# Optimization experiments

Hardware: AMD Instinct MI355X
Metric: run time of the kernel (lower is better)

Reference implementation:

```python
import jax, jax.numpy as jnp
import numpy as np

N = 50000
E = 800000
G = 8  # number of graphs
D_IN, D_H, D_OUT = 300, 128, 64


def _linear_params(key, d_out, d_in):
    k1, k2 = jax.random.split(key)
    s = 1.0 / np.sqrt(d_in)
    W = jax.random.uniform(k1, (d_out, d_in), minval=-s, maxval=s, dtype=jnp.float32)
    b = jax.random.uniform(k2, (d_out,), minval=-s, maxval=s, dtype=jnp.float32)
    return W, b


def setup_inputs() -> dict:
    key = jax.random.key(0)
    ks = jax.random.split(key, 10)
    x = jax.random.normal(ks[0], (N, D_IN), dtype=jnp.float32)
    edge_index = jax.random.randint(ks[1], (2, E), 0, N, dtype=jnp.int64)
    batch = jnp.sort(jax.random.randint(ks[2], (N,), 0, G, dtype=jnp.int64))
    W_emb, b_emb = _linear_params(ks[3], D_H, D_IN)
    # SAGEConv layer 0: lin_l (neighbors, with bias), lin_r (root, no bias)
    Wl0, bl0 = _linear_params(ks[4], D_H, D_H)
    Wr0, _ = _linear_params(ks[5], D_H, D_H)
    # SAGEConv layer 1
    Wl1, bl1 = _linear_params(ks[6], D_H, D_H)
    Wr1, _ = _linear_params(ks[7], D_H, D_H)
    W_att, b_att = _linear_params(ks[8], 1, D_H)
    W_out, b_out = _linear_params(ks[9], D_OUT, D_H)
    return {
        "x": x, "edge_index": edge_index, "batch": batch,
        "W_emb": W_emb, "b_emb": b_emb,
        "Wl0": Wl0, "bl0": bl0, "Wr0": Wr0,
        "Wl1": Wl1, "bl1": bl1, "Wr1": Wr1,
        "W_att": W_att, "b_att": b_att,
        "W_out": W_out, "b_out": b_out,
    }


def _sage_conv(h, src, dst, Wl, bl, Wr):
    # mean aggregation of source-node features onto destination nodes
    agg = jax.ops.segment_sum(h[src], dst, num_segments=N)  # [N, D_H]
    deg = jax.ops.segment_sum(jnp.ones((src.shape[0],), dtype=h.dtype), dst, num_segments=N)
    agg = agg / jnp.maximum(deg, 1.0)[:, None]
    return agg @ Wl.T + bl + h @ Wr.T


def reference(x, edge_index, batch, W_emb, b_emb, Wl0, bl0, Wr0, Wl1, bl1, Wr1,
              W_att, b_att, W_out, b_out):
    src, dst = edge_index[0], edge_index[1]
    h = x @ W_emb.T + b_emb                       # [N, D_H]
    h = jax.nn.relu(_sage_conv(h, src, dst, Wl0, bl0, Wr0))
    h = jax.nn.relu(_sage_conv(h, src, dst, Wl1, bl1, Wr1))
    # attention readout: softmax over ALL nodes (dim=0), as in original code
    scores = h @ W_att.T + b_att                  # [N, 1]
    weights = jax.nn.softmax(scores, axis=0)      # [N, 1]
    pooled = jax.ops.segment_sum(h * weights, batch, num_segments=G)  # [G, D_H]
    return pooled @ W_out.T + b_out               # [G, D_OUT]
```

## Files before the change

kernel.cpp:

```cpp
#include <hip/hip_runtime.h>
#include <math.h>

#define D_H 128

typedef __attribute__((ext_vector_type(8))) __bf16 bf16x8;
typedef __attribute__((ext_vector_type(4))) float f32x4;

__device__ __forceinline__ void split_bf16(float v, unsigned short& hi, unsigned short& lo) {
  unsigned int u = __float_as_uint(v);
  hi = (unsigned short)(u >> 16);
  float l = v - __uint_as_float(u & 0xffff0000u);
  lo = (unsigned short)(__float_as_uint(l) >> 16);
}

__device__ __forceinline__ float blo(unsigned int u) { return __uint_as_float(u << 16); }
__device__ __forceinline__ float bhi(unsigned int u) { return __uint_as_float(u & 0xffff0000u); }

__device__ __forceinline__ void pack_pair8(const float* xv, bf16x8& ah, bf16x8& al) {
  union { bf16x8 v; unsigned int u[4]; } H, L;
#pragma unroll
  for (int e = 0; e < 4; ++e) {
    unsigned int u0 = __float_as_uint(xv[2 * e]);
    unsigned int u1 = __float_as_uint(xv[2 * e + 1]);
    float l0 = xv[2 * e] - __uint_as_float(u0 & 0xffff0000u);
    float l1 = xv[2 * e + 1] - __uint_as_float(u1 & 0xffff0000u);
    H.u[e] = (u0 >> 16) | (u1 & 0xffff0000u);
    L.u[e] = (__float_as_uint(l0) >> 16) | (__float_as_uint(l1) & 0xffff0000u);
  }
  ah = H.v;
  al = L.v;
}

__device__ __forceinline__ void load_lds16(const void* g, void* l) {
  __builtin_amdgcn_global_load_lds((const __attribute__((address_space(1))) unsigned int*)g,
                                   (__attribute__((address_space(3))) unsigned int*)l,
                                   16, 0, 0);
}


__global__ __launch_bounds__(256) void k_histw(
    const int* __restrict__ dstv, int* __restrict__ bucketCnt, int E,
    const float* __restrict__ Wemb, const float* __restrict__ Wl0,
    const float* __restrict__ Wr0, const float* __restrict__ Wl1,
    const float* __restrict__ Wr1, unsigned short* __restrict__ WembP,
    unsigned short* __restrict__ P0l, unsigned short* __restrict__ P0r,
    unsigned short* __restrict__ P1l, unsigned short* __restrict__ P1r) {
  __shared__ int h[256];
  int t = threadIdx.x;
  h[t] = 0;
  __syncthreads();
  for (int i = blockIdx.x * 256 + t; i < E; i += gridDim.x * 256)
    atomicAdd(&h[dstv[i] >> 8], 1);

  int tid = blockIdx.x * 256 + t;
  const int EMB = 128 * 320;
  if (tid < EMB) {
    int o = tid / 320, k = tid - o * 320;
    float v = (k < 300) ? Wemb[o * 300 + k] : 0.f;
    unsigned short hh, ll;
    split_bf16(v, hh, ll);
    int sw = ((2 * k) ^ ((o & 7) << 4)) >> 1;
    WembP[o * 640 + sw] = hh;
    WembP[o * 640 + 320 + sw] = ll;
  } else if (tid < EMB + 4 * 16384) {
    int r = tid - EMB;
    int m = r >> 14;
    int i = r & 16383;
    int o = i >> 7, k = i & 127;
    const float* W = (m == 0) ? Wl0 : (m == 1) ? Wr0 : (m == 2) ? Wl1 : Wr1;
    unsigned short* P = (m == 0) ? P0l : (m == 1) ? P0r : (m == 2) ? P1l : P1r;
    unsigned short hh, ll;
    split_bf16(W[o * 128 + k], hh, ll);
    int sw = ((2 * k) ^ ((o & 7) << 4)) >> 1;
    P[o * 256 + sw] = hh;
    P[o * 256 + 128 + sw] = ll;
  }

  __syncthreads();
  if (h[t]) atomicAdd(&bucketCnt[t], h[t]);
}

__global__ __launch_bounds__(256) void k_bucketscan(const int* __restrict__ bucketCnt, int NB,
                                                    int* __restrict__ bucketBase,
                                                    int* __restrict__ cursor,
                                                    int* __restrict__ row_ptr, int N, int E) {
  __shared__ int s[256];
  int t = threadIdx.x;
  int v = (t < NB) ? bucketCnt[t] : 0;
  s[t] = v;
  __syncthreads();
  for (int off = 1; off < 256; off <<= 1) {
    int u = (t >= off) ? s[t - off] : 0;
    __syncthreads();
    s[t] += u;
    __syncthreads();
  }
  int excl = s[t] - v;
  if (t < NB) {
    bucketBase[t] = excl;
    cursor[t] = excl;
  }
  if (t == NB - 1) bucketBase[NB] = excl + v;
  if (t == 0) row_ptr[N] = E;
}

__global__ __launch_bounds__(256) void k_binscatter(const int* __restrict__ srcv,
                                                    const int* __restrict__ dstv,
                                                    int* __restrict__ cursor,
                                                    unsigned int* __restrict__ tmp, int E) {
  __shared__ int h[256];
  __shared__ int base[256];
  int t = threadIdx.x;
  int chunk = (E + gridDim.x - 1) / gridDim.x;
  int c0 = blockIdx.x * chunk;
  int c1 = min(c0 + chunk, E);
  int dst[16], src[16];
  h[t] = 0;
  __syncthreads();
#pragma unroll
  for (int p = 0; p < 16; ++p) {
    int i = c0 + p * 256 + t;
    if (i < c1) {
      dst[p] = dstv[i];
      src[p] = srcv[i];
      atomicAdd(&h[dst[p] >> 8], 1);
    } else {
      dst[p] = -1;
      src[p] = 0;
    }
  }
  __syncthreads();
  int cnt = h[t];
  __syncthreads();
  base[t] = cnt ? atomicAdd(&cursor[t], cnt) : 0;
  h[t] = 0;
  __syncthreads();
#pragma unroll
  for (int p = 0; p < 16; ++p) {
    if (dst[p] >= 0) {
      int b = dst[p] >> 8;
      int pos = base[b] + atomicAdd(&h[b], 1);
      tmp[pos] = (unsigned int)src[p] | ((unsigned int)(dst[p] & 255) << 16);
    }
  }
}

__global__ __launch_bounds__(256) void k_localcsr(const unsigned int* __restrict__ tmp,
                                                  const int* __restrict__ bucketBase,
                                                  int* __restrict__ row_ptr,
                                                  int* __restrict__ col, int N) {
  __shared__ int deg[256], rp[256], cur[256];
  int b = blockIdx.x, t = threadIdx.x;
  int s = bucketBase[b], e = bucketBase[b + 1];
  int epb = e - s;
  deg[t] = 0;
  __syncthreads();
  for (int i = t; i < epb; i += 256) atomicAdd(&deg[tmp[s + i] >> 16], 1);
  __syncthreads();
  int v = deg[t];
  rp[t] = v;
  __syncthreads();
  for (int off = 1; off < 256; off <<= 1) {
    int u = (t >= off) ? rp[t - off] : 0;
    __syncthreads();
    rp[t] += u;
    __syncthreads();
  }
  int excl = rp[t] - v;
  rp[t] = excl;
  cur[t] = 0;
  int gid = b * 256 + t;
  if (gid < N) row_ptr[gid] = s + excl;
  __syncthreads();
  for (int i = t; i < epb; i += 256) {
    unsigned int p = tmp[s + i];
    int dl = p >> 16;
    int pos = s + rp[dl] + atomicAdd(&cur[dl], 1);
    col[pos] = (int)(p & 0xffffu);
  }
}


__global__ __launch_bounds__(512, 4) void k_emb(const float* __restrict__ x,
                                                const unsigned short* __restrict__ Wp,
                                                const float* __restrict__ bias,
                                                unsigned short* __restrict__ P, int N) {
  __shared__ alignas(16) char sW[34048];
  int t = threadIdx.x, lane = t & 63, wave = t >> 6;
  int row0 = blockIdx.x * 128;
  int fr = lane & 15, q4 = lane >> 4;
  int X = (fr & 7) << 4;
  int row = row0 + wave * 16 + fr;
  if (row >= N) row = N - 1;
  const float* xrp = x + (size_t)row * 300;
  f32x4 acc[8] = {};
  float xb[2][8];

  auto loadx = [&](float* d, int c0) {
    if (c0 + 7 < 300) {
      float4 a = *(const float4*)(xrp + c0);
      float4 b = *(const float4*)(xrp + c0 + 4);
      d[0] = a.x; d[1] = a.y; d[2] = a.z; d[3] = a.w;
      d[4] = b.x; d[5] = b.y; d[6] = b.z; d[7] = b.w;
    } else {
#pragma unroll
      for (int e = 0; e < 8; ++e) d[e] = (c0 + e < 300) ? xrp[c0 + e] : 0.f;
    }
  };

  loadx(xb[0], q4 * 8);
#pragma unroll
  for (int kc = 0; kc < 5; ++kc) {
#pragma unroll
    for (int r = 0; r < 4; ++r) {
      int off = r * 8192 + wave * 1024;
      int offl = off + lane * 16;
      int c = offl >> 8;
      int w = offl & 255;
      const char* src = (const char*)Wp + (size_t)c * 1280 +
                        (w < 128 ? kc * 128 + w : 640 + kc * 128 + (w - 128));
      load_lds16(src, sW + off);
    }
    __syncthreads();
#pragma unroll
    for (int s = 0; s < 2; ++s) {
      int ks = kc * 2 + s;
      if (ks < 9) loadx(xb[(ks + 1) & 1], (ks + 1) * 32 + q4 * 8);
      bf16x8 ah, al;
      pack_pair8(xb[ks & 1], ah, al);
      int ko = (s * 64 + q4 * 16) ^ X;
#pragma unroll
      for (int j = 0; j < 8; ++j) {
        int c = j * 16 + fr;
        bf16x8 bh = *(const bf16x8*)(sW + c * 256 + ko);
        bf16x8 bl = *(const bf16x8*)(sW + c * 256 + 128 + ko);
        acc[j] = __builtin_amdgcn_mfma_f32_16x16x32_bf16(ah, bh, acc[j], 0, 0, 0);
        acc[j] = __builtin_amdgcn_mfma_f32_16x16x32_bf16(ah, bl, acc[j], 0, 0, 0);
        acc[j] = __builtin_amdgcn_mfma_f32_16x16x32_bf16(al, bh, acc[j], 0, 0, 0);
      }
    }
    __syncthreads();
  }

  float* T = (float*)sW;
#pragma unroll
  for (int ph = 0; ph < 2; ++ph) {
    if ((wave >> 2) == ph) {
      int wl = wave & 3;
#pragma unroll
      for (int j = 0; j < 8; ++j) {
        float b = bias[j * 16 + fr];
#pragma unroll
        for (int rg = 0; rg < 4; ++rg)
          T[(wl * 16 + q4 * 4 + rg) * 132 + j * 16 + fr] = acc[j][rg] + b;
      }
    }
    __syncthreads();
    int r = t >> 3, q = t & 7;
    float vals[16];
#pragma unroll
    for (int c = 0; c < 16; ++c) vals[c] = T[r * 132 + q * 16 + c];
    unsigned int hu[8], lu[8];
#pragma unroll
    for (int e = 0; e < 8; ++e) {
      unsigned int u0 = __float_as_uint(vals[2 * e]);
      unsigned int u1 = __float_as_uint(vals[2 * e + 1]);
      float l0 = vals[2 * e] - __uint_as_float(u0 & 0xffff0000u);
      float l1 = vals[2 * e + 1] - __uint_as_float(u1 & 0xffff0000u);
      hu[e] = (u0 >> 16) | (u1 & 0xffff0000u);
      lu[e] = (__float_as_uint(l0) >> 16) | (__float_as_uint(l1) & 0xffff0000u);
    }
    char* rowp = (char*)P + (size_t)(row0 + ph * 64 + r) * 512;
    *(uint4*)(rowp + q * 32) = make_uint4(hu[0], hu[1], hu[2], hu[3]);
    *(uint4*)(rowp + q * 32 + 16) = make_uint4(hu[4], hu[5], hu[6], hu[7]);
    *(uint4*)(rowp + 256 + q * 32) = make_uint4(lu[0], lu[1], lu[2], lu[3]);
    *(uint4*)(rowp + 256 + q * 32 + 16) = make_uint4(lu[4], lu[5], lu[6], lu[7]);
    __syncthreads();
  }
}


__global__ __launch_bounds__(512, 4) void k_conv(const unsigned short* __restrict__ Ap,
                                                 const unsigned short* __restrict__ Wl,
                                                 const unsigned short* __restrict__ Wr,
                                                 unsigned short* __restrict__ Ub,
                                                 float* __restrict__ V) {
  __shared__ alignas(16) char sW[34048];
  int t = threadIdx.x, lane = t & 63, wave = t >> 6;
  int wr2 = wave >> 1, wc = wave & 1;
  int row0 = blockIdx.x * 128;
  int fr = lane & 15, q4 = lane >> 4;
  int X = (fr & 7) << 4;

  f32x4 accU[2][4] = {};
  f32x4 accV[2][4] = {};

#pragma unroll
  for (int m = 0; m < 2; ++m) {
    const char* Wg = (const char*)(m ? Wr : Wl);
#pragma unroll
    for (int kc = 0; kc < 2; ++kc) {
#pragma unroll
      for (int r = 0; r < 4; ++r) {
        int off = r * 8192 + wave * 1024;
        int offl = off + lane * 16;
        int c = offl >> 8;
        int w = offl & 255;
        const char* src = Wg + (size_t)c * 512 +
                          (w < 128 ? kc * 128 + w : 256 + kc * 128 + (w - 128));
        load_lds16(src, sW + off);
      }
      __syncthreads();
#pragma unroll
      for (int s = 0; s < 2; ++s) {
        int ks = kc * 2 + s;
        bf16x8 ah[2], al[2];
#pragma unroll
        for (int i = 0; i < 2; ++i) {
          const char* ab =
              (const char*)Ap + (size_t)(row0 + wr2 * 32 + i * 16 + fr) * 512 + ks * 64 + q4 * 16;
          ah[i] = *(const bf16x8*)ab;
          al[i] = *(const bf16x8*)(ab + 256);
        }
        int ko = (s * 64 + q4 * 16) ^ X;
#pragma unroll
        for (int j = 0; j < 4; ++j) {
          int c = wc * 64 + j * 16 + fr;
          bf16x8 bh = *(const bf16x8*)(sW + c * 256 + ko);
          bf16x8 bl = *(const bf16x8*)(sW + c * 256 + 128 + ko);
#pragma unroll
          for (int i = 0; i < 2; ++i) {
            if (m == 0) {
              accU[i][j] = __builtin_amdgcn_mfma_f32_16x16x32_bf16(ah[i], bh, accU[i][j], 0, 0, 0);
              accU[i][j] = __builtin_amdgcn_mfma_f32_16x16x32_bf16(ah[i], bl, accU[i][j], 0, 0, 0);
              accU[i][j] = __builtin_amdgcn_mfma_f32_16x16x32_bf16(al[i], bh, accU[i][j], 0, 0, 0);
            } else {
              accV[i][j] = __builtin_amdgcn_mfma_f32_16x16x32_bf16(ah[i], bh, accV[i][j], 0, 0, 0);
              accV[i][j] = __builtin_amdgcn_mfma_f32_16x16x32_bf16(ah[i], bl, accV[i][j], 0, 0, 0);
              accV[i][j] = __builtin_amdgcn_mfma_f32_16x16x32_bf16(al[i], bh, accV[i][j], 0, 0, 0);
            }
          }
        }
      }
      __syncthreads();
    }
  }

#pragma unroll
  for (int i = 0; i < 2; ++i)
#pragma unroll
    for (int j = 0; j < 4; ++j)
#pragma unroll
      for (int rg = 0; rg < 4; ++rg)
        V[(size_t)(row0 + wr2 * 32 + i * 16 + q4 * 4 + rg) * D_H + wc * 64 + j * 16 + fr] =
            accV[i][j][rg];

  unsigned short* Tb = (unsigned short*)sW;
#pragma unroll
  for (int i = 0; i < 2; ++i)
#pragma unroll
    for (int j = 0; j < 4; ++j)
#pragma unroll
      for (int rg = 0; rg < 4; ++rg) {
        float v = accU[i][j][rg];
        unsigned int u = __float_as_uint(v);
        u += 0x7fffu + ((u >> 16) & 1);
        Tb[(wr2 * 32 + i * 16 + q4 * 4 + rg) * 132 + wc * 64 + j * 16 + fr] =
            (unsigned short)(u >> 16);
      }
  __syncthreads();
  int rr = t >> 2, q = t & 3;
  const unsigned short* src = Tb + rr * 132 + q * 32;
  uint4 o0 = *(const uint4*)src;
  uint4 o1 = *(const uint4*)(src + 8);
  uint4 o2 = *(const uint4*)(src + 16);
  uint4 o3 = *(const uint4*)(src + 24);
  char* drow = (char*)Ub + (size_t)(row0 + rr) * 256 + q * 64;
  *(uint4*)(drow) = o0;
  *(uint4*)(drow + 16) = o1;
  *(uint4*)(drow + 32) = o2;
  *(uint4*)(drow + 48) = o3;
}


__global__ __launch_bounds__(256) void k_aggfin1(const unsigned short* __restrict__ Ub,
                                                 const float* __restrict__ V,
                                                 const float* __restrict__ bias,
                                                 const int* __restrict__ row_ptr,
                                                 const int* __restrict__ col,
                                                 unsigned short* __restrict__ Hp, int N) {
  int wv = threadIdx.x >> 6;
  int wid = blockIdx.x * 4 + wv;
  int lane = threadIdx.x & 63;
  if (wid >= N) return;

  int half = lane >> 5;
  int dq = lane & 31;
  float a0 = 0.f, a1 = 0.f, a2 = 0.f, a3 = 0.f;

  const uint2* uvb = (const uint2*)Ub;
  int e0 = row_ptr[wid], e1 = row_ptr[wid + 1];
  int e = e0;
  for (; e + 8 <= e1; e += 8) {
    int s0 = col[e + half];
    int s1 = col[e + 2 + half];
    int s2 = col[e + 4 + half];
    int s3 = col[e + 6 + half];
    uint2 u0 = uvb[(size_t)s0 * 32 + dq];
    uint2 u1 = uvb[(size_t)s1 * 32 + dq];
    uint2 u2 = uvb[(size_t)s2 * 32 + dq];
    uint2 u3 = uvb[(size_t)s3 * 32 + dq];
    a0 += blo(u0.x) + blo(u1.x) + blo(u2.x) + blo(u3.x);
    a1 += bhi(u0.x) + bhi(u1.x) + bhi(u2.x) + bhi(u3.x);
    a2 += blo(u0.y) + blo(u1.y) + blo(u2.y) + blo(u3.y);
    a3 += bhi(u0.y) + bhi(u1.y) + bhi(u2.y) + bhi(u3.y);
  }
  for (; e + 2 <= e1; e += 2) {
    uint2 u = uvb[(size_t)col[e + half] * 32 + dq];
    a0 += blo(u.x);
    a1 += bhi(u.x);
    a2 += blo(u.y);
    a3 += bhi(u.y);
  }
  if (e < e1 && half == 0) {
    uint2 u = uvb[(size_t)col[e] * 32 + dq];
    a0 += blo(u.x);
    a1 += bhi(u.x);
    a2 += blo(u.y);
    a3 += bhi(u.y);
  }
  a0 += __shfl_xor(a0, 32);
  a1 += __shfl_xor(a1, 32);
  a2 += __shfl_xor(a2, 32);
  a3 += __shfl_xor(a3, 32);

  float inv = 1.f / fmaxf((float)(e1 - e0), 1.f);
  float4 vv = *(const float4*)(V + (size_t)wid * D_H + dq * 4);
  float4 bb = *(const float4*)(bias + dq * 4);
  float o0 = fmaxf(a0 * inv + vv.x + bb.x, 0.f);
  float o1 = fmaxf(a1 * inv + vv.y + bb.y, 0.f);
  float o2 = fmaxf(a2 * inv + vv.z + bb.z, 0.f);
  float o3 = fmaxf(a3 * inv + vv.w + bb.w, 0.f);

  unsigned int w0, w1;
  if (half == 0) {
    unsigned int x0 = __float_as_uint(o0), x1 = __float_as_uint(o1);
    unsigned int x2 = __float_as_uint(o2), x3 = __float_as_uint(o3);
    w0 = (x0 >> 16) | (x1 & 0xffff0000u);
    w1 = (x2 >> 16) | (x3 & 0xffff0000u);
  } else {
    unsigned short h, lq0, lq1, lq2, lq3;
    split_bf16(o0, h, lq0);
    split_bf16(o1, h, lq1);
    split_bf16(o2, h, lq2);
    split_bf16(o3, h, lq3);
    w0 = (unsigned int)lq0 | ((unsigned int)lq1 << 16);
    w1 = (unsigned int)lq2 | ((unsigned int)lq3 << 16);
  }
  *(uint2*)((char*)Hp + (size_t)wid * 512 + half * 256 + dq * 8) = make_uint2(w0, w1);
}


__global__ __launch_bounds__(256) void k_aggpool(const unsigned short* __restrict__ Ub,
                                                 const float* __restrict__ V,
                                                 const float* __restrict__ bias,
                                                 const int* __restrict__ row_ptr,
                                                 const int* __restrict__ col,
                                                 const int* __restrict__ batch,
                                                 const float* __restrict__ watt,
                                                 const float* __restrict__ batt,
                                                 float* __restrict__ slots,
                                                 float* __restrict__ zslot, int N) {
  __shared__ float pl[4][1024];
  __shared__ float zw[4];
  int t = threadIdx.x;
  int wv = t >> 6;
  int lane = t & 63;
  int half = lane >> 5;
  int dq = lane & 31;

  for (int i = lane; i < 1024; i += 64) pl[wv][i] = 0.f;
  float zacc = 0.f;

  const uint2* uvb = (const uint2*)Ub;
  float4 wat = *(const float4*)(watt + dq * 4);
  float bat = batt[0];
  float4 bb = *(const float4*)(bias + dq * 4);

  for (int i = 0; i < 4; ++i) {
    int wid = blockIdx.x * 16 + wv * 4 + i;
    if (wid >= N) break;
    float a0 = 0.f, a1 = 0.f, a2 = 0.f, a3 = 0.f;
    int e0 = row_ptr[wid], e1 = row_ptr[wid + 1];
    int e = e0;
    for (; e + 8 <= e1; e += 8) {
      int s0 = col[e + half];
      int s1 = col[e + 2 + half];
      int s2 = col[e + 4 + half];
      int s3 = col[e + 6 + half];
      uint2 u0 = uvb[(size_t)s0 * 32 + dq];
      uint2 u1 = uvb[(size_t)s1 * 32 + dq];
      uint2 u2 = uvb[(size_t)s2 * 32 + dq];
      uint2 u3 = uvb[(size_t)s3 * 32 + dq];
      a0 += blo(u0.x) + blo(u1.x) + blo(u2.x) + blo(u3.x);
      a1 += bhi(u0.x) + bhi(u1.x) + bhi(u2.x) + bhi(u3.x);
      a2 += blo(u0.y) + blo(u1.y) + blo(u2.y) + blo(u3.y);
      a3 += bhi(u0.y) + bhi(u1.y) + bhi(u2.y) + bhi(u3.y);
    }
    for (; e + 2 <= e1; e += 2) {
      uint2 u = uvb[(size_t)col[e + half] * 32 + dq];
      a0 += blo(u.x);
      a1 += bhi(u.x);
      a2 += blo(u.y);
      a3 += bhi(u.y);
    }
    if (e < e1 && half == 0) {
      uint2 u = uvb[(size_t)col[e] * 32 + dq];
      a0 += blo(u.x);
      a1 += bhi(u.x);
      a2 += blo(u.y);
      a3 += bhi(u.y);
    }
    a0 += __shfl_xor(a0, 32);
    a1 += __shfl_xor(a1, 32);
    a2 += __shfl_xor(a2, 32);
    a3 += __shfl_xor(a3, 32);

    float inv = 1.f / fmaxf((float)(e1 - e0), 1.f);
    float4 vv = *(const float4*)(V + (size_t)wid * D_H + dq * 4);
    float o0 = fmaxf(a0 * inv + vv.x + bb.x, 0.f);
    float o1 = fmaxf(a1 * inv + vv.y + bb.y, 0.f);
    float o2 = fmaxf(a2 * inv + vv.z + bb.z, 0.f);
    float o3 = fmaxf(a3 * inv + vv.w + bb.w, 0.f);

    float p = o0 * wat.x + o1 * wat.y + o2 * wat.z + o3 * wat.w;
#pragma unroll
    for (int off = 1; off < 32; off <<= 1) p += __shfl_xor(p, off);
    float wgt = __expf(p + bat);
    int b = batch[wid];
    if (half == 0) {
      float* pb = &pl[wv][b * 128 + dq * 4];
      pb[0] += wgt * o0;
      pb[1] += wgt * o1;
      pb[2] += wgt * o2;
      pb[3] += wgt * o3;
      if (dq == 0) zacc += wgt;
    }
  }
  if (lane == 0) zw[wv] = zacc;
  __syncthreads();
  float* slot = slots + (size_t)blockIdx.x * 1024;
  for (int i = t; i < 1024; i += 256)
    slot[i] = pl[0][i] + pl[1][i] + pl[2][i] + pl[3][i];
  if (t == 0) zslot[blockIdx.x] = zw[0] + zw[1] + zw[2] + zw[3];
}


__global__ __launch_bounds__(256) void k_poolred1(const float* __restrict__ slots,
                                                  int nslots, float* __restrict__ mid) {
  int r = blockIdx.x, t = threadIdx.x;
  float acc[4] = {0.f, 0.f, 0.f, 0.f};
  for (int s = r; s < nslots; s += 64) {
    const float* sp = slots + (size_t)s * 1024;
#pragma unroll
    for (int k = 0; k < 4; ++k) acc[k] += sp[t + k * 256];
  }
#pragma unroll
  for (int k = 0; k < 4; ++k) mid[(size_t)r * 1024 + t + k * 256] = acc[k];
}


__global__ __launch_bounds__(512) void k_poolred2(const float* __restrict__ mid,
                                                  const float* __restrict__ zslot, int nslots,
                                                  const float* __restrict__ Wout,
                                                  const float* __restrict__ bout,
                                                  float* __restrict__ out) {
  __shared__ float fin[1024];
  __shared__ float zs[512];
  int t = threadIdx.x;
  for (int i = t; i < 1024; i += 512) {
    float s = 0.f;
#pragma unroll
    for (int r = 0; r < 64; ++r) s += mid[(size_t)r * 1024 + i];
    fin[i] = s;
  }
  float z = 0.f;
  for (int i = t; i < nslots; i += 512) z += zslot[i];
  zs[t] = z;
  __syncthreads();
  for (int off = 256; off > 0; off >>= 1) {
    if (t < off) zs[t] += zs[t + off];
    __syncthreads();
  }
  float invZ = 1.f / zs[0];
  if (t < 512) {
    int g = t >> 6, oo = t & 63;
    const float* p = &fin[g * 128];
    const float* wr = Wout + (size_t)oo * 128;
    float acc = 0.f;
    for (int k = 0; k < 128; ++k) acc = fmaf(p[k], wr[k], acc);
    out[g * 64 + oo] = acc * invZ + bout[oo];
  }
}


extern "C" void kernel_launch(void* const* d_in, const int* in_sizes, int n_in,
                              void* d_out, int out_size, void* d_ws, size_t ws_size,
                              hipStream_t stream) {
  const float* x     = (const float*)d_in[0];
  const int*   ei    = (const int*)d_in[1];
  const int*   batch = (const int*)d_in[2];
  const float* W_emb = (const float*)d_in[3];
  const float* b_emb = (const float*)d_in[4];
  const float* Wl0   = (const float*)d_in[5];
  const float* bl0   = (const float*)d_in[6];
  const float* Wr0   = (const float*)d_in[7];
  const float* Wl1   = (const float*)d_in[8];
  const float* bl1   = (const float*)d_in[9];
  const float* Wr1   = (const float*)d_in[10];
  const float* W_att = (const float*)d_in[11];
  const float* b_att = (const float*)d_in[12];
  const float* W_out = (const float*)d_in[13];
  const float* b_out = (const float*)d_in[14];
  float* out = (float*)d_out;

  const int DIN = 300;
  int N = in_sizes[0] / DIN;
  int E = in_sizes[1] / 2;
  int Npad = (N + 127) & ~127;
  int NB = (N + 255) / 256;
  int nslots = (N + 15) / 16;

  char* wsp = (char*)d_ws;
  size_t off = 0;
  auto carve = [&](size_t bytes) -> void* {
    void* p = wsp + off;
    off += (bytes + 255) & ~(size_t)255;
    return p;
  };
  unsigned short* P  = (unsigned short*)carve((size_t)Npad * 512);
  unsigned short* Ub = (unsigned short*)carve((size_t)Npad * 256);
  float*          V  = (float*)carve((size_t)Npad * 512);
  unsigned short* WembP = (unsigned short*)carve((size_t)128 * 640 * 2);
  unsigned short* WP0l  = (unsigned short*)carve((size_t)128 * 256 * 2);
  unsigned short* WP0r  = (unsigned short*)carve((size_t)128 * 256 * 2);
  unsigned short* WP1l  = (unsigned short*)carve((size_t)128 * 256 * 2);
  unsigned short* WP1r  = (unsigned short*)carve((size_t)128 * 256 * 2);
  int*   colA    = (int*)carve((size_t)E * 4);
  unsigned int* tmpE = (unsigned int*)carve((size_t)E * 4);
  int*   row_ptr = (int*)carve((size_t)(N + 1) * 4);
  int*   bucketBase = (int*)carve((size_t)(NB + 1) * 4);
  int*   cursor     = (int*)carve((size_t)(NB + 1) * 4);
  float* slots   = (float*)carve((size_t)nslots * 1024 * 4);
  float* zslot   = (float*)carve((size_t)nslots * 4);
  float* mid     = (float*)carve((size_t)64 * 1024 * 4);
  int* bucketCnt = (int*)carve((size_t)(NB + 1) * 4);

  const int* srcv = ei;
  const int* dstv = ei + E;

  hipMemsetAsync(bucketCnt, 0, (size_t)(NB + 1) * 4, stream);
  k_histw<<<512, 256, 0, stream>>>(dstv, bucketCnt, E, W_emb, Wl0, Wr0, Wl1, Wr1,
                                   WembP, WP0l, WP0r, WP1l, WP1r);
  k_bucketscan<<<1, 256, 0, stream>>>(bucketCnt, NB, bucketBase, cursor, row_ptr, N, E);
  k_binscatter<<<256, 256, 0, stream>>>(srcv, dstv, cursor, tmpE, E);
  k_localcsr<<<NB, 256, 0, stream>>>(tmpE, bucketBase, row_ptr, colA, N);

  int gblocks = Npad / 128;
  k_emb<<<gblocks, 512, 0, stream>>>(x, WembP, b_emb, P, N);

  k_conv<<<gblocks, 512, 0, stream>>>(P, WP0l, WP0r, Ub, V);
  k_aggfin1<<<(N + 3) / 4, 256, 0, stream>>>(Ub, V, bl0, row_ptr, colA, P, N);
  k_conv<<<gblocks, 512, 0, stream>>>(P, WP1l, WP1r, Ub, V);
  k_aggpool<<<nslots, 256, 0, stream>>>(Ub, V, bl1, row_ptr, colA, batch,
                                        W_att, b_att, slots, zslot, N);

  k_poolred1<<<64, 256, 0, stream>>>(slots, nslots, mid);
  k_poolred2<<<1, 512, 0, stream>>>(mid, zslot, nslots, W_out, b_out, out);
}
```

Measured before the change: 233.2 us.

## Deepen gather unroll to 8 loads and fuse pool reductions via last-block counter

The neighbor gather loop in both aggregation kernels now issues eight independent index and feature loads per iteration instead of four, raising memory-level parallelism, and is shared through a macro. The two final pooling-reduction kernels become one kernel. Each block writes its partial sums, bumps an atomic counter, and the last block to arrive does the final reduction, softmax normalisation and output projection. This removes one launch and its gap, at the cost of more registers in the gather loop and a threadfence and atomic handshake, with the counter zeroed by the existing memset.

```diff
diff --git a/kernel.cpp b/kernel.cpp
--- a/kernel.cpp
+++ b/kernel.cpp
@@ -36,6 +36,43 @@
                                    (__attribute__((address_space(3))) unsigned int*)l,
                                    16, 0, 0);
 }
+
+#define GATHER_BODY(A0, A1, A2, A3)                                        \
+  {                                                                        \
+    int e = e0;                                                            \
+    for (; e + 16 <= e1; e += 16) {                                        \
+      int sc[8];                                                           \
+      uint2 uu[8];                                                         \
+      _Pragma("unroll") for (int k = 0; k < 8; ++k)                        \
+          sc[k] = col[e + 2 * k + half];                                   \
+      _Pragma("unroll") for (int k = 0; k < 8; ++k)                        \
+          uu[k] = uvb[(size_t)sc[k] * 32 + dq];                            \
+      _Pragma("unroll") for (int k = 0; k < 8; ++k) {                      \
+        A0 += blo(uu[k].x);                                                \
+        A1 += bhi(uu[k].x);                                                \
+        A2 += blo(uu[k].y);                                                \
+        A3 += bhi(uu[k].y);                                                \
+      }                                                                    \
+    }                                                                      \
+    for (; e + 2 <= e1; e += 2) {                                          \
+      uint2 u = uvb[(size_t)col[e + half] * 32 + dq];                      \
+      A0 += blo(u.x);                                                      \
+      A1 += bhi(u.x);                                                      \
+      A2 += blo(u.y);                                                      \
+      A3 += bhi(u.y);                                                      \
+    }                                                                      \
+    if (e < e1 && half == 0) {                                             \
+      uint2 u = uvb[(size_t)col[e] * 32 + dq];                             \
+      A0 += blo(u.x);                                                      \
+      A1 += bhi(u.x);                                                      \
+      A2 += blo(u.y);                                                      \
+      A3 += bhi(u.y);                                                      \
+    }                                                                      \
+    A0 += __shfl_xor(A0, 32);                                              \
+    A1 += __shfl_xor(A1, 32);                                              \
+    A2 += __shfl_xor(A2, 32);                                              \
+    A3 += __shfl_xor(A3, 32);                                              \
+  }
 
 
 __global__ __launch_bounds__(256) void k_histw(
@@ -400,39 +437,7 @@
 
   const uint2* uvb = (const uint2*)Ub;
   int e0 = row_ptr[wid], e1 = row_ptr[wid + 1];
-  int e = e0;
-  for (; e + 8 <= e1; e += 8) {
-    int s0 = col[e + half];
-    int s1 = col[e + 2 + half];
-    int s2 = col[e + 4 + half];
-    int s3 = col[e + 6 + half];
-    uint2 u0 = uvb[(size_t)s0 * 32 + dq];
-    uint2 u1 = uvb[(size_t)s1 * 32 + dq];
-    uint2 u2 = uvb[(size_t)s2 * 32 + dq];
-    uint2 u3 = uvb[(size_t)s3 * 32 + dq];
-    a0 += blo(u0.x) + blo(u1.x) + blo(u2.x) + blo(u3.x);
-    a1 += bhi(u0.x) + bhi(u1.x) + bhi(u2.x) + bhi(u3.x);
-    a2 += blo(u0.y) + blo(u1.y) + blo(u2.y) + blo(u3.y);
-    a3 += bhi(u0.y) + bhi(u1.y) + bhi(u2.y) + bhi(u3.y);
-  }
-  for (; e + 2 <= e1; e += 2) {
-    uint2 u = uvb[(size_t)col[e + half] * 32 + dq];
-    a0 += blo(u.x);
-    a1 += bhi(u.x);
-    a2 += blo(u.y);
-    a3 += bhi(u.y);
-  }
-  if (e < e1 && half == 0) {
-    uint2 u = uvb[(size_t)col[e] * 32 + dq];
-    a0 += blo(u.x);
-    a1 += bhi(u.x);
-    a2 += blo(u.y);
-    a3 += bhi(u.y);
-  }
-  a0 += __shfl_xor(a0, 32);
-  a1 += __shfl_xor(a1, 32);
-  a2 += __shfl_xor(a2, 32);
-  a3 += __shfl_xor(a3, 32);
+  GATHER_BODY(a0, a1, a2, a3)
 
   float inv = 1.f / fmaxf((float)(e1 - e0), 1.f);
   float4 vv = *(const float4*)(V + (size_t)wid * D_H + dq * 4);
@@ -492,39 +497,7 @@
     if (wid >= N) break;
     float a0 = 0.f, a1 = 0.f, a2 = 0.f, a3 = 0.f;
     int e0 = row_ptr[wid], e1 = row_ptr[wid + 1];
-    int e = e0;
-    for (; e + 8 <= e1; e += 8) {
-      int s0 = col[e + half];
-      int s1 = col[e + 2 + half];
-      int s2 = col[e + 4 + half];
-      int s3 = col[e + 6 + half];
-      uint2 u0 = uvb[(size_t)s0 * 32 + dq];
-      uint2 u1 = uvb[(size_t)s1 * 32 + dq];
-      uint2 u2 = uvb[(size_t)s2 * 32 + dq];
-      uint2 u3 = uvb[(size_t)s3 * 32 + dq];
-      a0 += blo(u0.x) + blo(u1.x) + blo(u2.x) + blo(u3.x);
-      a1 += bhi(u0.x) + bhi(u1.x) + bhi(u2.x) + bhi(u3.x);
-      a2 += blo(u0.y) + blo(u1.y) + blo(u2.y) + blo(u3.y);
-      a3 += bhi(u0.y) + bhi(u1.y) + bhi(u2.y) + bhi(u3.y);
-    }
-    for (; e + 2 <= e1; e += 2) {
-      uint2 u = uvb[(size_t)col[e + half] * 32 + dq];
-      a0 += blo(u.x);
-      a1 += bhi(u.x);
-      a2 += blo(u.y);
-      a3 += bhi(u.y);
-    }
-    if (e < e1 && half == 0) {
-      uint2 u = uvb[(size_t)col[e] * 32 + dq];
-      a0 += blo(u.x);
-      a1 += bhi(u.x);
-      a2 += blo(u.y);
-      a3 += bhi(u.y);
-    }
-    a0 += __shfl_xor(a0, 32);
-    a1 += __shfl_xor(a1, 32);
-    a2 += __shfl_xor(a2, 32);
-    a3 += __shfl_xor(a3, 32);
+    GATHER_BODY(a0, a1, a2, a3)
 
     float inv = 1.f / fmaxf((float)(e1 - e0), 1.f);
     float4 vv = *(const float4*)(V + (size_t)wid * D_H + dq * 4);
@@ -556,50 +529,58 @@
 }
 
 
-__global__ __launch_bounds__(256) void k_poolred1(const float* __restrict__ slots,
-                                                  int nslots, float* __restrict__ mid) {
+__global__ __launch_bounds__(256) void k_poolred(const float* __restrict__ slots,
+                                                 const float* __restrict__ zslot, int nslots,
+                                                 float* __restrict__ mid, float* __restrict__ zmid,
+                                                 int* __restrict__ ctr,
+                                                 const float* __restrict__ Wout,
+                                                 const float* __restrict__ bout,
+                                                 float* __restrict__ out) {
+  __shared__ int lastFlag;
+  __shared__ float fin[1024];
+  __shared__ float zs[256];
   int r = blockIdx.x, t = threadIdx.x;
   float acc[4] = {0.f, 0.f, 0.f, 0.f};
+  float z = 0.f;
   for (int s = r; s < nslots; s += 64) {
     const float* sp = slots + (size_t)s * 1024;
 #pragma unroll
     for (int k = 0; k < 4; ++k) acc[k] += sp[t + k * 256];
+    if (t == 0) z += zslot[s];
   }
 #pragma unroll
   for (int k = 0; k < 4; ++k) mid[(size_t)r * 1024 + t + k * 256] = acc[k];
-}
-
-
-__global__ __launch_bounds__(512) void k_poolred2(const float* __restrict__ mid,
-                                                  const float* __restrict__ zslot, int nslots,
-                                                  const float* __restrict__ Wout,
-                                                  const float* __restrict__ bout,
-                                                  float* __restrict__ out) {
-  __shared__ float fin[1024];
-  __shared__ float zs[512];
-  int t = threadIdx.x;
-  for (int i = t; i < 1024; i += 512) {
-    float s = 0.f;
-#pragma unroll
-    for (int r = 0; r < 64; ++r) s += mid[(size_t)r * 1024 + i];
-    fin[i] = s;
-  }
-  float z = 0.f;
-  for (int i = t; i < nslots; i += 512) z += zslot[i];
-  zs[t] = z;
-  __syncthreads();
-  for (int off = 256; off > 0; off >>= 1) {
-    if (t < off) zs[t] += zs[t + off];
-    __syncthreads();
-  }
-  float invZ = 1.f / zs[0];
-  if (t < 512) {
-    int g = t >> 6, oo = t & 63;
-    const float* p = &fin[g * 128];
-    const float* wr = Wout + (size_t)oo * 128;
-    float acc = 0.f;
-    for (int k = 0; k < 128; ++k) acc = fmaf(p[k], wr[k], acc);
-    out[g * 64 + oo] = acc * invZ + bout[oo];
+  if (t == 0) zmid[r] = z;
+
+  __threadfence();
+  __syncthreads();
+  if (t == 0) lastFlag = (atomicAdd(ctr, 1) == 63) ? 1 : 0;
+  __syncthreads();
+  if (lastFlag) {
+    __threadfence();
+    for (int i = t; i < 1024; i += 256) {
+      float s = 0.f;
+#pragma unroll
+      for (int q = 0; q < 64; ++q) s += mid[(size_t)q * 1024 + i];
+      fin[i] = s;
+    }
+    float zz = 0.f;
+    if (t < 64) zz = zmid[t];
+    zs[t] = zz;
+    __syncthreads();
+    for (int off = 128; off > 0; off >>= 1) {
+      if (t < off) zs[t] += zs[t + off];
+      __syncthreads();
+    }
+    float invZ = 1.f / zs[0];
+    for (int o = t; o < 512; o += 256) {
+      int g = o >> 6, oo = o & 63;
+      const float* p = &fin[g * 128];
+      const float* wr = Wout + (size_t)oo * 128;
+      float accd = 0.f;
+      for (int k = 0; k < 128; ++k) accd = fmaf(p[k], wr[k], accd);
+      out[g * 64 + oo] = accd * invZ + bout[oo];
+    }
   }
 }
 
@@ -654,12 +635,15 @@
   float* slots   = (float*)carve((size_t)nslots * 1024 * 4);
   float* zslot   = (float*)carve((size_t)nslots * 4);
   float* mid     = (float*)carve((size_t)64 * 1024 * 4);
-  int* bucketCnt = (int*)carve((size_t)(NB + 1) * 4);
+  float* zmid    = (float*)carve((size_t)64 * 4);
+  int* zbase = (int*)carve((size_t)(NB + 2) * 4);
+  int* bucketCnt = zbase;
+  int* ctr       = zbase + NB + 1;
 
   const int* srcv = ei;
   const int* dstv = ei + E;
 
-  hipMemsetAsync(bucketCnt, 0, (size_t)(NB + 1) * 4, stream);
+  hipMemsetAsync(zbase, 0, (size_t)(NB + 2) * 4, stream);
   k_histw<<<512, 256, 0, stream>>>(dstv, bucketCnt, E, W_emb, Wl0, Wr0, Wl1, Wr1,
                                    WembP, WP0l, WP0r, WP1l, WP1r);
   k_bucketscan<<<1, 256, 0, stream>>>(bucketCnt, NB, bucketBase, cursor, row_ptr, N, E);
@@ -675,6 +659,6 @@
   k_aggpool<<<nslots, 256, 0, stream>>>(Ub, V, bl1, row_ptr, colA, batch,
                                         W_att, b_att, slots, zslot, N);
 
-  k_poolred1<<<64, 256, 0, stream>>>(slots, nslots, mid);
-  k_poolred2<<<1, 512, 0, stream>>>(mid, zslot, nslots, W_out, b_out, out);
-}
+  k_poolred<<<64, 256, 0, stream>>>(slots, zslot, nslots, mid, zmid, ctr,
+                                    W_out, b_out, out);
+}
```

New measurement: 250.5 us. +7.4%, slower.
